# Performance work log

Hardware: AMD Instinct MI355X
Metric: run time of the kernel (lower is better)

## Reference

```python
import jax, jax.numpy as jnp
import numpy as np

N, D, H, E = 50000, 512, 8, 3200000
DK = D // H  # 64


def setup_inputs() -> dict:
    key = jax.random.key(0)
    ks = jax.random.split(key, 12)
    x = jax.random.normal(ks[0], (N, D), dtype=jnp.float32)
    row_index = jnp.sort(jax.random.randint(ks[1], (E,), 0, N))
    col_index = jax.random.randint(ks[2], (E,), 0, N)
    att_bias = jax.random.normal(ks[3], (H, E), dtype=jnp.float32)
    # xavier-uniform-ish linear params (bias zero per module init)
    lim = np.sqrt(6.0 / (D + D)).astype(np.float32)
    def w(k):
        return jax.random.uniform(k, (D, D), minval=-lim, maxval=lim, dtype=jnp.float32)
    return {
        "x": x, "row_index": row_index, "col_index": col_index, "att_bias": att_bias,
        "Wq": w(ks[4]), "bq": jnp.zeros((D,), jnp.float32),
        "Wk": w(ks[5]), "bk": jnp.zeros((D,), jnp.float32),
        "Wv": w(ks[6]), "bv": jnp.zeros((D,), jnp.float32),
        "Wo": w(ks[7]), "bo": jnp.zeros((D,), jnp.float32),
    }


def _proj(x, W, b):
    # nn.Linear then reshape(N, H, DK).permute(1,0,2) -> [H, N, DK]
    return (x @ W.T + b).reshape(x.shape[0], H, DK).transpose(1, 0, 2)


def reference(x, row_index, col_index, att_bias, Wq, bq, Wk, bk, Wv, bv, Wo, bo):
    q = _proj(x, Wq, bq) / jnp.sqrt(jnp.float32(DK))  # [H,N,DK]
    k = _proj(x, Wk, bk)
    v = _proj(x, Wv, bv)
    n = x.shape[0]
    # masked QK^T at sparse (row,col) entries + additive sparse bias -> [H,E]
    logits = jnp.einsum("hed,hed->he", q[:, row_index], k[:, col_index]) + att_bias
    # per-row (segment) softmax over CSR rows, vmapped over heads
    seg_max = jax.vmap(lambda l: jax.ops.segment_max(l, row_index, num_segments=n))(logits)  # [H,N]
    p = jnp.exp(logits - seg_max[:, row_index])
    denom = jax.vmap(lambda pe: jax.ops.segment_sum(pe, row_index, num_segments=n))(p)  # [H,N]
    att = p / denom[:, row_index]  # [H,E]
    # sparse att @ V : scatter-add weighted value rows
    y = jax.vmap(lambda a, vc: jax.ops.segment_sum(a[:, None] * vc, row_index, num_segments=n))(
        att, v[:, col_index]
    )  # [H,N,DK]
    y = y.transpose(1, 0, 2).reshape(n, H * DK)  # [N,D]
    return y @ Wo.T + bo
```

## Files before the change

### kernel.cpp

```cpp
#include <hip/hip_runtime.h>
#include <hip/hip_bf16.h>
#include <cstddef>
#include <cstdint>


typedef __attribute__((ext_vector_type(8))) short bf16x8;
typedef __attribute__((ext_vector_type(4))) float f32x4;

#define KQ_SCALE 25.4f
#define KQ_DEQ   0.03937007874f

#if __has_builtin(__builtin_amdgcn_sdot4)
__device__ __forceinline__ int SDOT4(int a, int b, int c) {
    return __builtin_amdgcn_sdot4(a, b, c, false);
}
#else
__device__ __forceinline__ int SDOT4(int a, int b, int c) {
#pragma unroll
    for (int i = 0; i < 4; ++i)
        c += (int)(signed char)((unsigned)a >> (8 * i)) *
             (int)(signed char)((unsigned)b >> (8 * i));
    return c;
}
#endif

__device__ __forceinline__ void gload_lds16(const void* g, const void* l) {
    __builtin_amdgcn_global_load_lds(
        (const __attribute__((address_space(1))) unsigned int*)g,
        (__attribute__((address_space(3))) unsigned int*)l, 16, 0, 0);
}

__device__ __forceinline__ float bflo(unsigned u) { return __uint_as_float(u << 16); }
__device__ __forceinline__ float bfhi(unsigned u) { return __uint_as_float(u & 0xffff0000u); }
__device__ __forceinline__ float ub(unsigned u, int i) {
    return (float)((u >> (i * 8)) & 0xffu);
}

__device__ __forceinline__ void storeT(float* p, size_t i, float v) { p[i] = v; }
__device__ __forceinline__ void storeT(__hip_bfloat16* p, size_t i, float v) {
    p[i] = __float2bfloat16(v);
}
__device__ __forceinline__ void storeT(unsigned char* p, size_t i, float v) {
    const float q = fmaf(v, KQ_SCALE, 128.0f);
    p[i] = (unsigned char)__float2uint_rn(fminf(fmaxf(q, 0.f), 255.f));
}
__device__ __forceinline__ void storeT(signed char* p, size_t i, float v) {
    p[i] = (signed char)__float2int_rn(fminf(fmaxf(v, -127.f), 127.f));
}

__global__ __launch_bounds__(256) void conv_f32_bf16(
    const float* __restrict__ s, __hip_bfloat16* __restrict__ d, int n) {
    const int i = (blockIdx.x * 256 + threadIdx.x) * 8;
    if (i >= n) return;
    const float4 a = *(const float4*)(s + i);
    const float4 b = *(const float4*)(s + i + 4);
    alignas(16) __hip_bfloat16 o[8] = {
        __float2bfloat16(a.x), __float2bfloat16(a.y),
        __float2bfloat16(a.z), __float2bfloat16(a.w),
        __float2bfloat16(b.x), __float2bfloat16(b.y),
        __float2bfloat16(b.z), __float2bfloat16(b.w)};
    *(uint4*)(d + i) = *(const uint4*)o;
}

__global__ void row_start_kernel(const int* __restrict__ row_index,
                                 int* __restrict__ row_start, int n_rows, int E) {
    const int n = blockIdx.x * blockDim.x + threadIdx.x;
    if (n > n_rows) return;
    int lo = 0, hi = E;
    while (lo < hi) {
        const int mid = (lo + hi) >> 1;
        if (row_index[mid] < n) lo = mid + 1; else hi = mid;
    }
    row_start[n] = lo;
}

__global__ __launch_bounds__(256) void quant_q_kernel(
    const __hip_bfloat16* __restrict__ qb, signed char* __restrict__ qi8,
    float* __restrict__ qdeq, int NH) {
    const int wid = blockIdx.x * 4 + (threadIdx.x >> 6);
    if (wid >= NH) return;
    const int lane = threadIdx.x & 63;
    const size_t off = (size_t)wid * 64 + lane;
    const float v = __bfloat162float(qb[off]);
    float a = fabsf(v);
#pragma unroll
    for (int st = 1; st < 64; st <<= 1) a = fmaxf(a, __shfl_xor(a, st, 64));
    const float scale = (a > 0.f) ? 127.0f / a : 0.f;
    qi8[off] = (signed char)__float2int_rn(v * scale);
    if (lane == 0) qdeq[wid] = a * (1.0f / 127.0f);
}

template <typename TO>
__global__ __launch_bounds__(256) void gemm_mfma_kernel(
    const short* __restrict__ A, const short* __restrict__ Bw,
    const float* __restrict__ bias, TO* __restrict__ C, int M, float scale) {
    __shared__ short As[128 * 32];
    __shared__ short Bs[128 * 32];
    const int t = threadIdx.x;
    const int w = t >> 6, l = t & 63;
    const int m0 = blockIdx.x * 128, n0 = blockIdx.y * 128;
    const int wrow = (w >> 1) * 64, wcol = (w & 1) * 64;
    const int fr = l & 15, fq = l >> 4;

    const int r0 = (w * 64 + l) >> 2, ko0 = ((w * 64 + l) & 3) * 8;
    int gmA0 = m0 + r0;      if (gmA0 >= M) gmA0 = M - 1;
    int gmA1 = m0 + r0 + 64; if (gmA1 >= M) gmA1 = M - 1;
    const int gnB0 = n0 + r0, gnB1 = n0 + r0 + 64;

    f32x4 acc[4][4];
#pragma unroll
    for (int mi = 0; mi < 4; ++mi)
#pragma unroll
        for (int ni = 0; ni < 4; ++ni) acc[mi][ni] = (f32x4){0.f, 0.f, 0.f, 0.f};

    for (int k0 = 0; k0 < 512; k0 += 32) {
        __syncthreads();
        gload_lds16(A + (size_t)gmA0 * 512 + k0 + ko0, As + w * 512);
        gload_lds16(A + (size_t)gmA1 * 512 + k0 + ko0, As + 2048 + w * 512);
        gload_lds16(Bw + (size_t)gnB0 * 512 + k0 + ko0, Bs + w * 512);
        gload_lds16(Bw + (size_t)gnB1 * 512 + k0 + ko0, Bs + 2048 + w * 512);
        __syncthreads();

        bf16x8 af[4], bfr[4];
#pragma unroll
        for (int mi = 0; mi < 4; ++mi)
            af[mi] = *(const bf16x8*)(As + (wrow + mi * 16 + fr) * 32 + fq * 8);
#pragma unroll
        for (int ni = 0; ni < 4; ++ni)
            bfr[ni] = *(const bf16x8*)(Bs + (wcol + ni * 16 + fr) * 32 + fq * 8);
#pragma unroll
        for (int mi = 0; mi < 4; ++mi)
#pragma unroll
            for (int ni = 0; ni < 4; ++ni)
                acc[mi][ni] = __builtin_amdgcn_mfma_f32_16x16x32_bf16(
                    af[mi], bfr[ni], acc[mi][ni], 0, 0, 0);
    }

#pragma unroll
    for (int mi = 0; mi < 4; ++mi)
#pragma unroll
        for (int ni = 0; ni < 4; ++ni)
#pragma unroll
            for (int r = 0; r < 4; ++r) {
                const int gr = m0 + wrow + mi * 16 + fq * 4 + r;
                if (gr < M) {
                    const int gc = n0 + wcol + ni * 16 + fr;
                    storeT(C, (size_t)gr * 512 + gc, (acc[mi][ni][r] + bias[gc]) * scale);
                }
            }
}

__global__ __launch_bounds__(256) void sparse_attn_kernel(
    const signed char* __restrict__ qi8, const float* __restrict__ qdeq,
    const signed char* __restrict__ kq, const unsigned char* __restrict__ vq,
    const int* __restrict__ col_index, const float* __restrict__ att_bias,
    const int* __restrict__ row_start, __hip_bfloat16* __restrict__ yout, int E) {
    const int n = blockIdx.x;
    const int w = threadIdx.x >> 6;
    const int lane = threadIdx.x & 63;
    const int g = lane & 7;
    const int j = lane >> 3;
    const int hA = 2 * w + (g >> 2);
    const int dim0 = (g & 3) * 16;
    const int e0 = row_start[n], e1 = row_start[n + 1];

    const int4 qu = *(const int4*)(qi8 + (size_t)n * 512 + hA * 64 + dim0);
    const float dsc = qdeq[(size_t)n * 8 + hA] * KQ_DEQ;

    const float* biasH = att_bias + (size_t)hA * (size_t)E;
    const unsigned pairoff = (unsigned)(w * 128 + g * 16);

    float acc[16];
#pragma unroll
    for (int i = 0; i < 16; ++i) acc[i] = 0.f;
    float s_lane = 0.f;

    if (e0 < e1) {
        const int e1m1 = e1 - 1;
        for (int base = e0; base < e1; base += 16) {
            const int eA = base + j, eB = base + 8 + j;
            const int ecA = min(eA, e1m1), ecB = min(eB, e1m1);
            const int cA = col_index[ecA], cB = col_index[ecB];
            const unsigned coA = ((unsigned)cA << 9) + pairoff;
            const unsigned coB = ((unsigned)cB << 9) + pairoff;
            const int4 kuA = *(const int4*)(kq + coA);
            const uint4 vuA = *(const uint4*)(vq + coA);
            const int4 kuB = *(const int4*)(kq + coB);
            const uint4 vuB = *(const uint4*)(vq + coB);
            const float bvA = biasH[ecA];
            const float bvB = biasH[ecB];

            int a0 = 0, a1 = 0, b0 = 0, b1 = 0;
            a0 = SDOT4(qu.x, kuA.x, a0);
            a1 = SDOT4(qu.y, kuA.y, a1);
            b0 = SDOT4(qu.x, kuB.x, b0);
            b1 = SDOT4(qu.y, kuB.y, b1);
            a0 = SDOT4(qu.z, kuA.z, a0);
            a1 = SDOT4(qu.w, kuA.w, a1);
            b0 = SDOT4(qu.z, kuB.z, b0);
            b1 = SDOT4(qu.w, kuB.w, b1);
            int idA = a0 + a1, idB = b0 + b1;
            idA += __shfl_xor(idA, 1, 64);
            idB += __shfl_xor(idB, 1, 64);
            idA += __shfl_xor(idA, 2, 64);
            idB += __shfl_xor(idB, 2, 64);
            const float lgA = fmaf((float)idA, dsc, bvA);
            const float lgB = fmaf((float)idB, dsc, bvB);
            const float pA = (eA < e1) ? __expf(lgA) : 0.f;
            const float pB = (eB < e1) ? __expf(lgB) : 0.f;
            s_lane += pA + pB;

            {
                const unsigned* uA = (const unsigned*)&vuA;
                const unsigned* uB = (const unsigned*)&vuB;
#pragma unroll
                for (int i = 0; i < 4; ++i)
#pragma unroll
                    for (int b = 0; b < 4; ++b) {
                        acc[4 * i + b] = fmaf(pA, ub(uA[i], b), acc[4 * i + b]);
                        acc[4 * i + b] = fmaf(pB, ub(uB[i], b), acc[4 * i + b]);
                    }
            }
        }
    }

#pragma unroll
    for (int st = 8; st < 64; st <<= 1) s_lane += __shfl_xor(s_lane, st, 64);
#pragma unroll
    for (int i = 0; i < 16; ++i) {
#pragma unroll
        for (int st = 8; st < 64; st <<= 1) acc[i] += __shfl_xor(acc[i], st, 64);
    }

    float y0 = acc[0], y1 = acc[1];
#pragma unroll
    for (int t = 1; t < 8; ++t) {
        y0 = (j == t) ? acc[2 * t] : y0;
        y1 = (j == t) ? acc[2 * t + 1] : y1;
    }
    const size_t orow = (size_t)n * 512 + hA * 64 + dim0 + 2 * j;
    if (s_lane > 0.f) {
        const float inv = 1.0f / s_lane;
        yout[orow]     = __float2bfloat16(fmaf(KQ_DEQ, y0 * inv, -128.0f * KQ_DEQ));
        yout[orow + 1] = __float2bfloat16(fmaf(KQ_DEQ, y1 * inv, -128.0f * KQ_DEQ));
    } else {
        yout[orow]     = __float2bfloat16(0.f);
        yout[orow + 1] = __float2bfloat16(0.f);
    }
}

extern "C" void kernel_launch(void* const* d_in, const int* in_sizes, int n_in,
                              void* d_out, int out_size, void* d_ws, size_t ws_size,
                              hipStream_t stream) {
    const float* x         = (const float*)d_in[0];
    const int*   row_index = (const int*)d_in[1];
    const int*   col_index = (const int*)d_in[2];
    const float* att_bias  = (const float*)d_in[3];
    const float* Wq = (const float*)d_in[4];
    const float* bq = (const float*)d_in[5];
    const float* Wk = (const float*)d_in[6];
    const float* bk = (const float*)d_in[7];
    const float* Wv = (const float*)d_in[8];
    const float* bv = (const float*)d_in[9];
    const float* Wo = (const float*)d_in[10];
    const float* bo = (const float*)d_in[11];
    float* out = (float*)d_out;

    const int N = in_sizes[0] / 512;
    const int E = in_sizes[1];
    const int WN = 512 * 512;

    char* ws = (char*)d_ws;
    const size_t nb = (size_t)N * 512 * sizeof(__hip_bfloat16);
    const size_t b8 = (size_t)N * 512;
    const size_t wb = (size_t)WN * sizeof(__hip_bfloat16);
    __hip_bfloat16* xb  = (__hip_bfloat16*)(ws);
    __hip_bfloat16* qb  = (__hip_bfloat16*)(ws + nb);
    signed char*    kq8 = (signed char*)(ws + 2 * nb);
    unsigned char*  vq8 = (unsigned char*)(ws + 2 * nb + b8);
    signed char*    qi8 = (signed char*)(ws + 2 * nb + 2 * b8);
    __hip_bfloat16* wqb = (__hip_bfloat16*)(ws + 2 * nb + 3 * b8);
    __hip_bfloat16* wkb = (__hip_bfloat16*)(ws + 2 * nb + 3 * b8 + wb);
    __hip_bfloat16* wvb = (__hip_bfloat16*)(ws + 2 * nb + 3 * b8 + 2 * wb);
    __hip_bfloat16* wob = (__hip_bfloat16*)(ws + 2 * nb + 3 * b8 + 3 * wb);
    float* qdeq = (float*)(ws + 2 * nb + 3 * b8 + 4 * wb);
    int* row_start = (int*)(ws + 2 * nb + 3 * b8 + 4 * wb + (size_t)N * 8 * 4);

    conv_f32_bf16<<<(N * 512 / 8 + 255) / 256, 256, 0, stream>>>(x, xb, N * 512);
    conv_f32_bf16<<<(WN / 8 + 255) / 256, 256, 0, stream>>>(Wq, wqb, WN);
    conv_f32_bf16<<<(WN / 8 + 255) / 256, 256, 0, stream>>>(Wk, wkb, WN);
    conv_f32_bf16<<<(WN / 8 + 255) / 256, 256, 0, stream>>>(Wv, wvb, WN);
    conv_f32_bf16<<<(WN / 8 + 255) / 256, 256, 0, stream>>>(Wo, wob, WN);

    row_start_kernel<<<(N + 1 + 255) / 256, 256, 0, stream>>>(row_index, row_start, N, E);

    const dim3 gg((N + 127) / 128, 4), gb(256);
    gemm_mfma_kernel<__hip_bfloat16><<<gg, gb, 0, stream>>>(
        (const short*)xb, (const short*)wqb, bq, qb, N, 0.125f);
    gemm_mfma_kernel<signed char><<<gg, gb, 0, stream>>>(
        (const short*)xb, (const short*)wkb, bk, kq8, N, KQ_SCALE);
    gemm_mfma_kernel<unsigned char><<<gg, gb, 0, stream>>>(
        (const short*)xb, (const short*)wvb, bv, vq8, N, 1.0f);

    quant_q_kernel<<<(N * 8 + 3) / 4, 256, 0, stream>>>(qb, qi8, qdeq, N * 8);

    sparse_attn_kernel<<<N, 256, 0, stream>>>(
        qi8, qdeq, kq8, vq8, col_index, att_bias, row_start, xb , E);

    gemm_mfma_kernel<float><<<gg, gb, 0, stream>>>(
        (const short*)xb, (const short*)wob, bo, out, N, 1.0f);
}
```

Before: 831.4 us.

## Fuse per-head Q int8 quantization into Q GEMM epilogue and unroll attention edges

```diff
diff --git a/kernel.cpp b/kernel.cpp
--- a/kernel.cpp
+++ b/kernel.cpp
@@ -74,21 +74,6 @@
     row_start[n] = lo;
 }
 
-__global__ __launch_bounds__(256) void quant_q_kernel(
-    const __hip_bfloat16* __restrict__ qb, signed char* __restrict__ qi8,
-    float* __restrict__ qdeq, int NH) {
-    const int wid = blockIdx.x * 4 + (threadIdx.x >> 6);
-    if (wid >= NH) return;
-    const int lane = threadIdx.x & 63;
-    const size_t off = (size_t)wid * 64 + lane;
-    const float v = __bfloat162float(qb[off]);
-    float a = fabsf(v);
-#pragma unroll
-    for (int st = 1; st < 64; st <<= 1) a = fmaxf(a, __shfl_xor(a, st, 64));
-    const float scale = (a > 0.f) ? 127.0f / a : 0.f;
-    qi8[off] = (signed char)__float2int_rn(v * scale);
-    if (lane == 0) qdeq[wid] = a * (1.0f / 127.0f);
-}
 
 template <typename TO>
 __global__ __launch_bounds__(256) void gemm_mfma_kernel(
@@ -148,6 +133,81 @@
                     storeT(C, (size_t)gr * 512 + gc, (acc[mi][ni][r] + bias[gc]) * scale);
                 }
             }
+}
+
+__global__ __launch_bounds__(256) void gemm_mfma_quantq_kernel(
+    const short* __restrict__ A, const short* __restrict__ Bw,
+    const float* __restrict__ bias, signed char* __restrict__ qi8,
+    float* __restrict__ qdeq, int M, float scale) {
+    __shared__ short As[128 * 32];
+    __shared__ short Bs[128 * 32];
+    const int t = threadIdx.x;
+    const int w = t >> 6, l = t & 63;
+    const int m0 = blockIdx.x * 128, n0 = blockIdx.y * 128;
+    const int wrow = (w >> 1) * 64, wcol = (w & 1) * 64;
+    const int fr = l & 15, fq = l >> 4;
+
+    const int r0 = (w * 64 + l) >> 2, ko0 = ((w * 64 + l) & 3) * 8;
+    int gmA0 = m0 + r0;      if (gmA0 >= M) gmA0 = M - 1;
+    int gmA1 = m0 + r0 + 64; if (gmA1 >= M) gmA1 = M - 1;
+    const int gnB0 = n0 + r0, gnB1 = n0 + r0 + 64;
+
+    f32x4 acc[4][4];
+#pragma unroll
+    for (int mi = 0; mi < 4; ++mi)
+#pragma unroll
+        for (int ni = 0; ni < 4; ++ni) acc[mi][ni] = (f32x4){0.f, 0.f, 0.f, 0.f};
+
+    for (int k0 = 0; k0 < 512; k0 += 32) {
+        __syncthreads();
+        gload_lds16(A + (size_t)gmA0 * 512 + k0 + ko0, As + w * 512);
+        gload_lds16(A + (size_t)gmA1 * 512 + k0 + ko0, As + 2048 + w * 512);
+        gload_lds16(Bw + (size_t)gnB0 * 512 + k0 + ko0, Bs + w * 512);
+        gload_lds16(Bw + (size_t)gnB1 * 512 + k0 + ko0, Bs + 2048 + w * 512);
+        __syncthreads();
+
+        bf16x8 af[4], bfr[4];
+#pragma unroll
+        for (int mi = 0; mi < 4; ++mi)
+            af[mi] = *(const bf16x8*)(As + (wrow + mi * 16 + fr) * 32 + fq * 8);
+#pragma unroll
+        for (int ni = 0; ni < 4; ++ni)
+            bfr[ni] = *(const bf16x8*)(Bs + (wcol + ni * 16 + fr) * 32 + fq * 8);
+#pragma unroll
+        for (int mi = 0; mi < 4; ++mi)
+#pragma unroll
+            for (int ni = 0; ni < 4; ++ni)
+                acc[mi][ni] = __builtin_amdgcn_mfma_f32_16x16x32_bf16(
+                    af[mi], bfr[ni], acc[mi][ni], 0, 0, 0);
+    }
+
+    const int head = (n0 + wcol) >> 6;
+#pragma unroll
+    for (int mi = 0; mi < 4; ++mi)
+#pragma unroll
+        for (int r = 0; r < 4; ++r) {
+            const int gr = m0 + wrow + mi * 16 + fq * 4 + r;
+            float v[4];
+            float a = 0.f;
+#pragma unroll
+            for (int ni = 0; ni < 4; ++ni) {
+                const int gc = n0 + wcol + ni * 16 + fr;
+                v[ni] = (acc[mi][ni][r] + bias[gc]) * scale;
+                a = fmaxf(a, fabsf(v[ni]));
+            }
+#pragma unroll
+            for (int st = 1; st < 16; st <<= 1) a = fmaxf(a, __shfl_xor(a, st, 64));
+            const float sc = (a > 0.f) ? 127.0f / a : 0.f;
+            if (gr < M) {
+#pragma unroll
+                for (int ni = 0; ni < 4; ++ni) {
+                    const int gc = n0 + wcol + ni * 16 + fr;
+                    qi8[(size_t)gr * 512 + gc] =
+                        (signed char)__float2int_rn(v[ni] * sc);
+                }
+                if (fr == 0) qdeq[(size_t)gr * 8 + head] = a * (1.0f / 127.0f);
+            }
+        }
 }
 
 __global__ __launch_bounds__(256) void sparse_attn_kernel(
@@ -177,49 +237,52 @@
 
     if (e0 < e1) {
         const int e1m1 = e1 - 1;
-        for (int base = e0; base < e1; base += 16) {
-            const int eA = base + j, eB = base + 8 + j;
-            const int ecA = min(eA, e1m1), ecB = min(eB, e1m1);
-            const int cA = col_index[ecA], cB = col_index[ecB];
-            const unsigned coA = ((unsigned)cA << 9) + pairoff;
-            const unsigned coB = ((unsigned)cB << 9) + pairoff;
-            const int4 kuA = *(const int4*)(kq + coA);
-            const uint4 vuA = *(const uint4*)(vq + coA);
-            const int4 kuB = *(const int4*)(kq + coB);
-            const uint4 vuB = *(const uint4*)(vq + coB);
-            const float bvA = biasH[ecA];
-            const float bvB = biasH[ecB];
-
-            int a0 = 0, a1 = 0, b0 = 0, b1 = 0;
-            a0 = SDOT4(qu.x, kuA.x, a0);
-            a1 = SDOT4(qu.y, kuA.y, a1);
-            b0 = SDOT4(qu.x, kuB.x, b0);
-            b1 = SDOT4(qu.y, kuB.y, b1);
-            a0 = SDOT4(qu.z, kuA.z, a0);
-            a1 = SDOT4(qu.w, kuA.w, a1);
-            b0 = SDOT4(qu.z, kuB.z, b0);
-            b1 = SDOT4(qu.w, kuB.w, b1);
-            int idA = a0 + a1, idB = b0 + b1;
-            idA += __shfl_xor(idA, 1, 64);
-            idB += __shfl_xor(idB, 1, 64);
-            idA += __shfl_xor(idA, 2, 64);
-            idB += __shfl_xor(idB, 2, 64);
-            const float lgA = fmaf((float)idA, dsc, bvA);
-            const float lgB = fmaf((float)idB, dsc, bvB);
-            const float pA = (eA < e1) ? __expf(lgA) : 0.f;
-            const float pB = (eB < e1) ? __expf(lgB) : 0.f;
-            s_lane += pA + pB;
-
-            {
-                const unsigned* uA = (const unsigned*)&vuA;
-                const unsigned* uB = (const unsigned*)&vuB;
+        for (int base = e0; base < e1; base += 32) {
+            int ec[4]; unsigned co[4];
+#pragma unroll
+            for (int t = 0; t < 4; ++t) {
+                ec[t] = min(base + t * 8 + j, e1m1);
+                co[t] = ((unsigned)col_index[ec[t]] << 9) + pairoff;
+            }
+            int4 ku[4]; uint4 vu[4]; float bv[4];
+#pragma unroll
+            for (int t = 0; t < 4; ++t) {
+                ku[t] = *(const int4*)(kq + co[t]);
+                vu[t] = *(const uint4*)(vq + co[t]);
+                bv[t] = biasH[ec[t]];
+            }
+
+            int id[4];
+#pragma unroll
+            for (int t = 0; t < 4; ++t) {
+                int a0 = 0, a1 = 0;
+                a0 = SDOT4(qu.x, ku[t].x, a0);
+                a1 = SDOT4(qu.y, ku[t].y, a1);
+                a0 = SDOT4(qu.z, ku[t].z, a0);
+                a1 = SDOT4(qu.w, ku[t].w, a1);
+                id[t] = a0 + a1;
+            }
+#pragma unroll
+            for (int t = 0; t < 4; ++t) {
+                id[t] += __shfl_xor(id[t], 1, 64);
+                id[t] += __shfl_xor(id[t], 2, 64);
+            }
+            float p[4];
+#pragma unroll
+            for (int t = 0; t < 4; ++t)
+                p[t] = (base + t * 8 + j < e1)
+                           ? __expf(fmaf((float)id[t], dsc, bv[t]))
+                           : 0.f;
+            s_lane += (p[0] + p[1]) + (p[2] + p[3]);
+
+#pragma unroll
+            for (int t = 0; t < 4; ++t) {
+                const unsigned* u = (const unsigned*)&vu[t];
 #pragma unroll
                 for (int i = 0; i < 4; ++i)
 #pragma unroll
-                    for (int b = 0; b < 4; ++b) {
-                        acc[4 * i + b] = fmaf(pA, ub(uA[i], b), acc[4 * i + b]);
-                        acc[4 * i + b] = fmaf(pB, ub(uB[i], b), acc[4 * i + b]);
-                    }
+                    for (int b = 0; b < 4; ++b)
+                        acc[4 * i + b] = fmaf(p[t], ub(u[i], b), acc[4 * i + b]);
             }
         }
     }
@@ -275,16 +338,15 @@
     const size_t b8 = (size_t)N * 512;
     const size_t wb = (size_t)WN * sizeof(__hip_bfloat16);
     __hip_bfloat16* xb  = (__hip_bfloat16*)(ws);
-    __hip_bfloat16* qb  = (__hip_bfloat16*)(ws + nb);
-    signed char*    kq8 = (signed char*)(ws + 2 * nb);
-    unsigned char*  vq8 = (unsigned char*)(ws + 2 * nb + b8);
-    signed char*    qi8 = (signed char*)(ws + 2 * nb + 2 * b8);
-    __hip_bfloat16* wqb = (__hip_bfloat16*)(ws + 2 * nb + 3 * b8);
-    __hip_bfloat16* wkb = (__hip_bfloat16*)(ws + 2 * nb + 3 * b8 + wb);
-    __hip_bfloat16* wvb = (__hip_bfloat16*)(ws + 2 * nb + 3 * b8 + 2 * wb);
-    __hip_bfloat16* wob = (__hip_bfloat16*)(ws + 2 * nb + 3 * b8 + 3 * wb);
-    float* qdeq = (float*)(ws + 2 * nb + 3 * b8 + 4 * wb);
-    int* row_start = (int*)(ws + 2 * nb + 3 * b8 + 4 * wb + (size_t)N * 8 * 4);
+    signed char*    kq8 = (signed char*)(ws + nb);
+    unsigned char*  vq8 = (unsigned char*)(ws + nb + b8);
+    signed char*    qi8 = (signed char*)(ws + nb + 2 * b8);
+    __hip_bfloat16* wqb = (__hip_bfloat16*)(ws + nb + 3 * b8);
+    __hip_bfloat16* wkb = (__hip_bfloat16*)(ws + nb + 3 * b8 + wb);
+    __hip_bfloat16* wvb = (__hip_bfloat16*)(ws + nb + 3 * b8 + 2 * wb);
+    __hip_bfloat16* wob = (__hip_bfloat16*)(ws + nb + 3 * b8 + 3 * wb);
+    float* qdeq = (float*)(ws + nb + 3 * b8 + 4 * wb);
+    int* row_start = (int*)(ws + nb + 3 * b8 + 4 * wb + (size_t)N * 8 * 4);
 
     conv_f32_bf16<<<(N * 512 / 8 + 255) / 256, 256, 0, stream>>>(x, xb, N * 512);
     conv_f32_bf16<<<(WN / 8 + 255) / 256, 256, 0, stream>>>(Wq, wqb, WN);
@@ -295,15 +357,13 @@
     row_start_kernel<<<(N + 1 + 255) / 256, 256, 0, stream>>>(row_index, row_start, N, E);
 
     const dim3 gg((N + 127) / 128, 4), gb(256);
-    gemm_mfma_kernel<__hip_bfloat16><<<gg, gb, 0, stream>>>(
-        (const short*)xb, (const short*)wqb, bq, qb, N, 0.125f);
+    gemm_mfma_quantq_kernel<<<gg, gb, 0, stream>>>(
+        (const short*)xb, (const short*)wqb, bq, qi8, qdeq, N, 0.125f);
     gemm_mfma_kernel<signed char><<<gg, gb, 0, stream>>>(
         (const short*)xb, (const short*)wkb, bk, kq8, N, KQ_SCALE);
     gemm_mfma_kernel<unsigned char><<<gg, gb, 0, stream>>>(
         (const short*)xb, (const short*)wvb, bv, vq8, N, 1.0f);
 
-    quant_q_kernel<<<(N * 8 + 3) / 4, 256, 0, stream>>>(qb, qi8, qdeq, N * 8);
-
     sparse_attn_kernel<<<N, 256, 0, stream>>>(
         qi8, qdeq, kq8, vq8, col_index, att_bias, row_start, xb , E);
 
```

After: 757.3 us. 8.9% less time.
